# Optimization experiments

Hardware: AMD Instinct MI355X
Metric: run time of the kernel (lower is better)

## Reference

```python
import jax, jax.numpy as jnp
import numpy as np

N_NODES = 100000

def setup_inputs() -> dict:
    key = jax.random.key(0)
    k1, k2, k3 = jax.random.split(key, 3)
    x = jax.random.normal(k1, (N_NODES, 64), dtype=jnp.float32)
    edge_index = jax.random.randint(k2, (2, 1600000), 0, N_NODES, dtype=jnp.int64)
    edge_weights = jax.random.uniform(k3, (1600000,), dtype=jnp.float32)
    weight = jnp.ones((1,), dtype=jnp.float32)  # MyConv.weight, reset to 1
    return {"x": x, "edge_index": edge_index, "edge_weights": edge_weights, "weight": weight}

def reference(x, edge_index, edge_weights, weight):
    src = edge_index[0]  # x_j (source nodes, messages flow source->target)
    dst = edge_index[1]  # aggregation target i
    # message: edge_weight * x_j ; aggregate: scatter-add at dst
    msgs = edge_weights[:, None] * x[src]              # [E, D]
    agg = jax.ops.segment_sum(msgs, dst, num_segments=N_NODES)  # [N, D]
    # conv1: x + weight * aggregate, then relu (Encoder only applies conv1)
    return jax.nn.relu(x + weight * agg)
```

## Files before the change

kernel.cpp:

```cpp
#include <hip/hip_runtime.h>

constexpr int N_NODES = 100000;
constexpr int D       = 64;
constexpr int N_EDGES = 1600000;
constexpr int OUT_N4  = N_NODES * D / 4;

constexpr int NPB   = 128;
constexpr int NBUCK = (N_NODES + NPB - 1) / NPB;
constexpr int BCAP  = 2560;
constexpr int CPAD  = 32;
constexpr int CHUNK = 4096;
constexpr int PB    = (N_EDGES + CHUNK - 1) / CHUNK;
constexpr int PTHREADS = 1024;

__global__ void detect_kernel(const unsigned long long* __restrict__ ei,
                              int* __restrict__ flag) {
    if (blockIdx.x == 0 && threadIdx.x == 0) {
        int is64 = 1;
#pragma unroll
        for (int i = 0; i < 8; ++i)
            if (ei[i] >= (unsigned long long)N_NODES) is64 = 0;
        *flag = is64;
    }
}

__device__ __forceinline__ int load_idx(const void* ei_raw, int flag, long long pos) {
    if (flag) return (int)((const long long*)ei_raw)[pos];
    return ((const int*)ei_raw)[pos];
}

__device__ __forceinline__ unsigned short bf16rne(float f) {
    unsigned u = __float_as_uint(f);
    unsigned r = (u + 0x7fffu + ((u >> 16) & 1u)) >> 16;
    return (unsigned short)r;
}
__device__ __forceinline__ float bf16f(unsigned short u) {
    return __uint_as_float(((unsigned)u) << 16);
}

__global__ void prep_kernel(const float4* __restrict__ x4,
                            ushort4* __restrict__ x16v,
                            int* __restrict__ cursor) {
    int i = blockIdx.x * blockDim.x + threadIdx.x;
    int stride = gridDim.x * blockDim.x;
    for (int j = i; j < NBUCK * CPAD; j += stride) cursor[j] = 0;
    for (; i < OUT_N4; i += stride) {
        float4 v = x4[i];
        ushort4 o;
        o.x = bf16rne(v.x); o.y = bf16rne(v.y);
        o.z = bf16rne(v.z); o.w = bf16rne(v.w);
        x16v[i] = o;
    }
}

__global__ __launch_bounds__(PTHREADS) void part_kernel(
        const void* __restrict__ ei_raw,
        const float* __restrict__ ew,
        const int* __restrict__ flag,
        int* __restrict__ cursor,
        int2* __restrict__ slots) {
    __shared__ int hist[NBUCK];
    __shared__ int fill[NBUCK];
    __shared__ int runbase[NBUCK];
    int tid = threadIdx.x;
    for (int t = tid; t < NBUCK; t += PTHREADS) { hist[t] = 0; fill[t] = 0; }
    __syncthreads();

    int f = *flag;
    long long base = (long long)blockIdx.x * CHUNK;

    for (int it = 0; it < CHUNK / PTHREADS; ++it) {
        long long e = base + it * PTHREADS + tid;
        if (e < N_EDGES) {
            int dst = load_idx(ei_raw, f, (long long)N_EDGES + e);
            atomicAdd(&hist[dst >> 7], 1);
        }
    }
    __syncthreads();

    for (int t = tid; t < NBUCK; t += PTHREADS) {
        int c = hist[t];
        runbase[t] = (c > 0) ? atomicAdd(&cursor[t * CPAD], c) : 0;
    }
    __syncthreads();

    for (int it = 0; it < CHUNK / PTHREADS; ++it) {
        long long e = base + it * PTHREADS + tid;
        if (e < N_EDGES) {
            int src = load_idx(ei_raw, f, e);
            int dst = load_idx(ei_raw, f, (long long)N_EDGES + e);
            int b  = dst >> 7;
            int dl = dst & (NPB - 1);
            int r  = atomicAdd(&fill[b], 1);
            int idx = runbase[b] + r;
            if (idx < BCAP) {
                int2 rec;
                rec.x = (src << 7) | dl;
                rec.y = __float_as_int(ew[e]);
                slots[(long long)b * BCAP + idx] = rec;
            }
        }
    }
}

__global__ __launch_bounds__(256) void sort_bucket_kernel(
        const int* __restrict__ cursor,
        const int2* __restrict__ slots,
        int2* __restrict__ sorted,
        int2* __restrict__ oc ) {
    __shared__ int  hist[NPB];
    __shared__ int  scn[NPB];
    __shared__ int  fill[NPB];
    __shared__ int2 raw[BCAP];
    __shared__ int2 srt[BCAP];

    int tid = threadIdx.x;
    int b   = blockIdx.x;

    if (tid < NPB) { hist[tid] = 0; fill[tid] = 0; }
    __syncthreads();

    int cnt = cursor[b * CPAD];
    if (cnt > BCAP) cnt = BCAP;
    const int2* sb = slots + (long long)b * BCAP;

    for (int i = tid; i < cnt; i += 256) {
        int2 r = sb[i];
        raw[i] = r;
        atomicAdd(&hist[r.x & (NPB - 1)], 1);
    }
    __syncthreads();

    if (tid < NPB) scn[tid] = hist[tid];
    __syncthreads();
    for (int off = 1; off < NPB; off <<= 1) {
        int v = 0;
        if (tid < NPB && tid >= off) v = scn[tid - off];
        __syncthreads();
        if (tid < NPB) scn[tid] += v;
        __syncthreads();
    }

    if (tid < NPB) {
        int node = b * NPB + tid;
        if (node < N_NODES) {
            int2 v;
            v.x = b * BCAP + (scn[tid] - hist[tid]);
            v.y = hist[tid];
            oc[node] = v;
        }
    }
    __syncthreads();

    for (int i = tid; i < cnt; i += 256) {
        int2 r = raw[i];
        int dl = r.x & (NPB - 1);
        int pos = (scn[dl] - hist[dl]) + atomicAdd(&fill[dl], 1);
        srt[pos] = r;
    }
    __syncthreads();

    int2* ob = sorted + (long long)b * BCAP;
    for (int i = tid; i < cnt; i += 256) ob[i] = srt[i];
}

__global__ __launch_bounds__(256) void gather_csr_kernel(
        const unsigned short* __restrict__ x16,
        const int2* __restrict__ oc,
        const int2* __restrict__ sorted,
        const float* __restrict__ weight,
        float* __restrict__ out) {
    int lane = threadIdx.x & 63;
    int node = __builtin_amdgcn_readfirstlane(
        (int)((blockIdx.x * blockDim.x + threadIdx.x) >> 6));
    if (node >= N_NODES) return;

    int2 v = oc[node];
    int beg = __builtin_amdgcn_readfirstlane(v.x);
    int cnt = __builtin_amdgcn_readfirstlane(v.y);
    const int2* s = sorted + beg;

    float a0 = 0.f, a1 = 0.f, a2 = 0.f, a3 = 0.f;
    int k = 0;
    for (; k + 8 <= cnt; k += 8) {
        int2 r0 = s[k];     int2 r1 = s[k + 1];
        int2 r2 = s[k + 2]; int2 r3 = s[k + 3];
        int2 r4 = s[k + 4]; int2 r5 = s[k + 5];
        int2 r6 = s[k + 6]; int2 r7 = s[k + 7];
        float x0 = bf16f(x16[(r0.x >> 7) * D + lane]);
        float x1 = bf16f(x16[(r1.x >> 7) * D + lane]);
        float x2 = bf16f(x16[(r2.x >> 7) * D + lane]);
        float x3 = bf16f(x16[(r3.x >> 7) * D + lane]);
        float x4 = bf16f(x16[(r4.x >> 7) * D + lane]);
        float x5 = bf16f(x16[(r5.x >> 7) * D + lane]);
        float x6 = bf16f(x16[(r6.x >> 7) * D + lane]);
        float x7 = bf16f(x16[(r7.x >> 7) * D + lane]);
        a0 += __int_as_float(r0.y) * x0;
        a1 += __int_as_float(r1.y) * x1;
        a2 += __int_as_float(r2.y) * x2;
        a3 += __int_as_float(r3.y) * x3;
        a0 += __int_as_float(r4.y) * x4;
        a1 += __int_as_float(r5.y) * x5;
        a2 += __int_as_float(r6.y) * x6;
        a3 += __int_as_float(r7.y) * x7;
    }
    for (; k + 2 <= cnt; k += 2) {
        int2 r0 = s[k];
        int2 r1 = s[k + 1];
        a0 += __int_as_float(r0.y) * bf16f(x16[(r0.x >> 7) * D + lane]);
        a1 += __int_as_float(r1.y) * bf16f(x16[(r1.x >> 7) * D + lane]);
    }
    if (k < cnt) {
        int2 r0 = s[k];
        a0 += __int_as_float(r0.y) * bf16f(x16[(r0.x >> 7) * D + lane]);
    }
    float acc = (a0 + a1) + (a2 + a3);

    float r = bf16f(x16[node * D + lane]) + weight[0] * acc;
    out[node * D + lane] = fmaxf(r, 0.f);
}

__global__ void init_out_kernel(const float4* __restrict__ x4,
                                float4* __restrict__ out4) {
    int i = blockIdx.x * blockDim.x + threadIdx.x;
    int stride = gridDim.x * blockDim.x;
    for (; i < OUT_N4; i += stride) out4[i] = x4[i];
}

__global__ __launch_bounds__(256) void scatter_atomic_kernel(
        const float* __restrict__ x,
        const void* __restrict__ ei_raw,
        const float* __restrict__ ew,
        const float* __restrict__ weight,
        const int* __restrict__ flag,
        float* __restrict__ out) {
    long long gid = (long long)blockIdx.x * blockDim.x + threadIdx.x;
    int e = (int)(gid >> 6);
    int d = (int)(gid & 63);
    if (e >= N_EDGES) return;
    int f = *flag;
    int src = load_idx(ei_raw, f, e);
    int dst = load_idx(ei_raw, f, (long long)N_EDGES + e);
    float w = weight[0] * ew[e];
    atomicAdd(&out[dst * D + d], w * x[src * D + d]);
}

__global__ void relu_kernel(float4* __restrict__ out4) {
    int i = blockIdx.x * blockDim.x + threadIdx.x;
    int stride = gridDim.x * blockDim.x;
    for (; i < OUT_N4; i += stride) {
        float4 v = out4[i];
        v.x = fmaxf(v.x, 0.0f);
        v.y = fmaxf(v.y, 0.0f);
        v.z = fmaxf(v.z, 0.0f);
        v.w = fmaxf(v.w, 0.0f);
        out4[i] = v;
    }
}

extern "C" void kernel_launch(void* const* d_in, const int* in_sizes, int n_in,
                              void* d_out, int out_size, void* d_ws, size_t ws_size,
                              hipStream_t stream) {
    const float* x      = (const float*)d_in[0];
    const void*  ei     = d_in[1];
    const float* ew     = (const float*)d_in[2];
    const float* weight = (const float*)d_in[3];
    float* out = (float*)d_out;

    char* w = (char*)d_ws;
    auto align256 = [](size_t v) { return (v + 255) & ~(size_t)255; };

    size_t off = 0;
    int* flag = (int*)(w + off);        off = align256(off + 4);
    int* cursor = (int*)(w + off);      off = align256(off + (size_t)NBUCK * CPAD * 4);
    int2* oc = (int2*)(w + off);        off = align256(off + (size_t)N_NODES * 8);
    unsigned short* x16 = (unsigned short*)(w + off);
                                        off = align256(off + (size_t)N_NODES * D * 2);
    int2* slots = (int2*)(w + off);     off = align256(off + (size_t)NBUCK * BCAP * 8);
    int2* sorted = (int2*)(w + off);    off = align256(off + (size_t)NBUCK * BCAP * 8);
    size_t needed = off;

    detect_kernel<<<1, 64, 0, stream>>>((const unsigned long long*)ei, flag);

    if (ws_size >= needed) {
        prep_kernel<<<2048, 256, 0, stream>>>((const float4*)x, (ushort4*)x16, cursor);
        part_kernel<<<PB, PTHREADS, 0, stream>>>(ei, ew, flag, cursor, slots);
        sort_bucket_kernel<<<NBUCK, 256, 0, stream>>>(cursor, slots, sorted, oc);
        gather_csr_kernel<<<(N_NODES * 64 + 255) / 256, 256, 0, stream>>>(
            x16, oc, sorted, weight, out);
    } else {
        init_out_kernel<<<2048, 256, 0, stream>>>((const float4*)x, (float4*)out);
        long long total = (long long)N_EDGES * 64;
        scatter_atomic_kernel<<<(int)((total + 255) / 256), 256, 0, stream>>>(
            x, ei, ew, weight, flag, out);
        relu_kernel<<<2048, 256, 0, stream>>>((float4*)out);
    }
}
```

Measured before the change: 104.1 us.

## Stage partitioned edges in LDS sorted by bucket before coalesced global write

The partition kernel now loads each edge once into registers instead of reading the indices twice. It builds a block-local histogram and prefix scan, places records into a bucket-sorted shared-memory staging array, and then writes them out contiguously so that global stores to the slots array are coalesced rather than scattered. In exchange it uses more LDS (a CHUNK-sized int2 and ushort buffer) and a serial Hillis-Steele scan with many barriers, which may lower occupancy. NBUCK (782) must fit in PTHREADS for the scan to be correct.

```diff
diff --git a/kernel.cpp b/kernel.cpp
--- a/kernel.cpp
+++ b/kernel.cpp
@@ -9,9 +9,10 @@
 constexpr int NBUCK = (N_NODES + NPB - 1) / NPB;
 constexpr int BCAP  = 2560;
 constexpr int CPAD  = 32;
-constexpr int CHUNK = 4096;
+constexpr int PTHREADS = 1024;
+constexpr int EPT   = 4;
+constexpr int CHUNK = PTHREADS * EPT;
 constexpr int PB    = (N_EDGES + CHUNK - 1) / CHUNK;
-constexpr int PTHREADS = 1024;
 
 __global__ void detect_kernel(const unsigned long long* __restrict__ ei,
                               int* __restrict__ flag) {
@@ -59,9 +60,14 @@
         const int* __restrict__ flag,
         int* __restrict__ cursor,
         int2* __restrict__ slots) {
-    __shared__ int hist[NBUCK];
-    __shared__ int fill[NBUCK];
-    __shared__ int runbase[NBUCK];
+    __shared__ int  hist[NBUCK];
+    __shared__ int  scn[PTHREADS];
+    __shared__ int  localbase[NBUCK];
+    __shared__ int  runbase[NBUCK];
+    __shared__ int  fill[NBUCK];
+    __shared__ int2 srt[CHUNK];
+    __shared__ unsigned short aux[CHUNK];
+
     int tid = threadIdx.x;
     for (int t = tid; t < NBUCK; t += PTHREADS) { hist[t] = 0; fill[t] = 0; }
     __syncthreads();
@@ -69,37 +75,58 @@
     int f = *flag;
     long long base = (long long)blockIdx.x * CHUNK;
 
-    for (int it = 0; it < CHUNK / PTHREADS; ++it) {
-        long long e = base + it * PTHREADS + tid;
-        if (e < N_EDGES) {
-            int dst = load_idx(ei_raw, f, (long long)N_EDGES + e);
-            atomicAdd(&hist[dst >> 7], 1);
-        }
-    }
-    __syncthreads();
-
-    for (int t = tid; t < NBUCK; t += PTHREADS) {
-        int c = hist[t];
-        runbase[t] = (c > 0) ? atomicAdd(&cursor[t * CPAD], c) : 0;
-    }
-    __syncthreads();
-
-    for (int it = 0; it < CHUNK / PTHREADS; ++it) {
+    int  rb[EPT];
+    int2 rrec[EPT];
+#pragma unroll
+    for (int it = 0; it < EPT; ++it) {
         long long e = base + it * PTHREADS + tid;
         if (e < N_EDGES) {
             int src = load_idx(ei_raw, f, e);
             int dst = load_idx(ei_raw, f, (long long)N_EDGES + e);
-            int b  = dst >> 7;
-            int dl = dst & (NPB - 1);
-            int r  = atomicAdd(&fill[b], 1);
-            int idx = runbase[b] + r;
-            if (idx < BCAP) {
-                int2 rec;
-                rec.x = (src << 7) | dl;
-                rec.y = __float_as_int(ew[e]);
-                slots[(long long)b * BCAP + idx] = rec;
-            }
+            int b = dst >> 7;
+            rb[it] = b;
+            rrec[it].x = (src << 7) | (dst & (NPB - 1));
+            rrec[it].y = __float_as_int(ew[e]);
+            atomicAdd(&hist[b], 1);
+        } else {
+            rb[it] = -1;
         }
+    }
+    __syncthreads();
+
+    scn[tid] = (tid < NBUCK) ? hist[tid] : 0;
+    __syncthreads();
+    for (int off = 1; off < PTHREADS; off <<= 1) {
+        int v = (tid >= off) ? scn[tid - off] : 0;
+        __syncthreads();
+        scn[tid] += v;
+        __syncthreads();
+    }
+    if (tid < NBUCK) {
+        localbase[tid] = scn[tid] - hist[tid];
+        int c = hist[tid];
+        runbase[tid] = (c > 0) ? atomicAdd(&cursor[tid * CPAD], c) : 0;
+    }
+    __syncthreads();
+
+#pragma unroll
+    for (int it = 0; it < EPT; ++it) {
+        int b = rb[it];
+        if (b >= 0) {
+            int p = localbase[b] + atomicAdd(&fill[b], 1);
+            srt[p] = rrec[it];
+            aux[p] = (unsigned short)b;
+        }
+    }
+    __syncthreads();
+
+    int total = scn[NBUCK - 1];
+    for (int i = tid; i < total; i += PTHREADS) {
+        int b = aux[i];
+        int g = runbase[b] + (i - localbase[b]);
+        if (g < (int)((long long)b * BCAP + BCAP) - (int)((long long)b * BCAP)) {}
+        long long gpos = (long long)b * BCAP + g;
+        if (g < BCAP) slots[gpos] = srt[i];
     }
 }
 
```

Result: faster. 98.48 us (-5.4%).
